# Kernel optimization log

Measured on AMD Instinct MI355X. Metric: run time of the kernel, lower is better.

## Reference

```python
import jax, jax.numpy as jnp
import numpy as np

C = 256  # image_channels == mask_channels == output_channels

def setup_inputs() -> dict:
    key = jax.random.key(0)
    ks = jax.random.split(key, 10)
    B, H, W = 16, 48, 48
    s = 0.02
    return {
        "image_feat": jax.random.normal(ks[0], (B, C, H, W), jnp.float32),
        "mask_feat": jax.random.normal(ks[1], (B, C, H, W), jnp.float32),
        "Wq": jax.random.normal(ks[2], (C, C), jnp.float32) * s,
        "bq": jnp.zeros((C,), jnp.float32),
        "Wk": jax.random.normal(ks[3], (C, C), jnp.float32) * s,
        "bk": jnp.zeros((C,), jnp.float32),
        "Wv": jax.random.normal(ks[4], (C, C), jnp.float32) * s,
        "bv": jnp.zeros((C,), jnp.float32),
        "Wo": jax.random.normal(ks[5], (C, C), jnp.float32) * s,
        "bo": jnp.zeros((C,), jnp.float32),
    }

def reference(image_feat, mask_feat, Wq, bq, Wk, bk, Wv, bv, Wo, bo):
    B, Cc, H, W = image_feat.shape
    N = H * W
    img = image_feat.reshape(B, Cc, N)   # [B, C, N]
    msk = mask_feat.reshape(B, Cc, N)
    # 1x1 convs == per-pixel linear over channels
    q = jnp.einsum('oc,bcn->bon', Wq, msk) + bq[None, :, None]
    k = jnp.einsum('oc,bcn->bon', Wk, img) + bk[None, :, None]
    v = jnp.einsum('oc,bcn->bon', Wv, img) + bv[None, :, None]
    scale = Cc ** (-0.5)
    # attn[b, n, m] = <q[:, n], k[:, m]>
    attn = jnp.einsum('bcn,bcm->bnm', q, k) * scale
    attn = jax.nn.softmax(attn, axis=-1)
    # attended[b, c, n] = sum_m v[b, c, m] * attn[b, n, m]
    av = jnp.einsum('bcm,bnm->bcn', v, attn)
    out = jnp.einsum('oc,bcn->bon', Wo, av) + bo[None, :, None]
    return image_feat + out.reshape(B, Cc, H, W)
```

## Files before the change

kernel.cpp:

```cpp
#include <hip/hip_runtime.h>

#define NBATCH 16
#define CCH 256
#define NTOK 2304

typedef __attribute__((ext_vector_type(8))) short bf16x8;
typedef __attribute__((ext_vector_type(4))) short bf16x4v;
typedef __attribute__((ext_vector_type(4))) float f32x4;

__device__ __forceinline__ short f2bf(float x){
  unsigned u = __builtin_bit_cast(unsigned, x);
  u = u + 0x7FFFu + ((u >> 16) & 1u);
  return (short)(u >> 16);
}
__device__ __forceinline__ float bf2f(short h){
  unsigned u = ((unsigned)(unsigned short)h) << 16;
  return __builtin_bit_cast(float, u);
}

__device__ __forceinline__ void gld_lds16(const short* g, short* l){
  __builtin_amdgcn_global_load_lds((const __attribute__((address_space(1))) void*)g,
                                   (__attribute__((address_space(3))) void*)l, 16, 0, 0);
}

__global__ __launch_bounds__(256) void cw_kernel(const float* __restrict__ Wq, const float* __restrict__ Wk,
                                                 const float* __restrict__ Wv, const float* __restrict__ Wo,
                                                 short* __restrict__ out){
  int idx = blockIdx.x * 256 + threadIdx.x;
  int which = idx >> 14;
  int off = idx & 16383;
  const float* src = which==0 ? Wq : which==1 ? Wk : which==2 ? Wv : Wo;
  float4 v = ((const float4*)src)[off];
  bf16x4v pk = { f2bf(v.x), f2bf(v.y), f2bf(v.z), f2bf(v.w) };
  *(bf16x4v*)(out + ((size_t)which << 16) + ((size_t)off << 2)) = pk;
}

__global__ __launch_bounds__(256) void prep_kernel(const float* __restrict__ img, const float* __restrict__ msk,
                                                   short* __restrict__ imgT, short* __restrict__ mskT){
  int zz = blockIdx.z; int b = zz >> 1; int which = zz & 1;
  const float* src = (which ? msk : img) + (size_t)b * CCH * NTOK;
  short* dst = (which ? mskT : imgT) + (size_t)b * NTOK * CCH;
  int n0 = blockIdx.x * 64, c0 = blockIdx.y * 64;
  __shared__ __align__(16) short tile[64][72];
  int tid = threadIdx.x;
  int r = tid >> 2, g = tid & 3;
  const float* p = src + (size_t)(c0 + r) * NTOK + n0 + 16 * g;
  #pragma unroll
  for (int q4 = 0; q4 < 4; q4++){
    float4 v = *(const float4*)(p + 4 * q4);
    tile[16*g + 4*q4 + 0][r] = f2bf(v.x);
    tile[16*g + 4*q4 + 1][r] = f2bf(v.y);
    tile[16*g + 4*q4 + 2][r] = f2bf(v.z);
    tile[16*g + 4*q4 + 3][r] = f2bf(v.w);
  }
  __syncthreads();
  short* qp = dst + (size_t)(n0 + r) * CCH + c0 + 16 * g;
  *(bf16x8*)qp = *(const bf16x8*)&tile[r][16*g];
  *(bf16x8*)(qp + 8) = *(const bf16x8*)&tile[r][16*g + 8];
}

__device__ __forceinline__ void gemm128(const short* __restrict__ Ablk, const short* __restrict__ Bblk,
                                        short* As, short* Bs, f32x4 (&acc)[4][4]){
  const int tid = threadIdx.x;
  const int l = tid & 63, w = tid >> 6;
  const int l15 = l & 15, lhi = l >> 4;
  const int wi = w >> 1, wj = w & 1;
  const int srow = tid >> 3, scs = tid & 7;
  const f32x4 z4 = {0.f, 0.f, 0.f, 0.f};
  #pragma unroll
  for (int mt = 0; mt < 4; mt++)
    #pragma unroll
    for (int nt = 0; nt < 4; nt++) acc[mt][nt] = z4;

  #pragma unroll 1
  for (int kt = 0; kt < 4; kt++){
    const int k0 = kt * 64;
    bf16x8 ra[4], rb[4];
    #pragma unroll
    for (int p = 0; p < 4; p++){
      const int row = p * 32 + srow;
      ra[p] = *(const bf16x8*)(Ablk + (size_t)row * CCH + k0 + 8 * scs);
      rb[p] = *(const bf16x8*)(Bblk + (size_t)row * CCH + k0 + 8 * scs);
    }
    __syncthreads();
    #pragma unroll
    for (int p = 0; p < 4; p++){
      const int row = p * 32 + srow;
      const int sw = (scs ^ (row & 7)) << 3;
      *(bf16x8*)(As + row * 64 + sw) = ra[p];
      *(bf16x8*)(Bs + row * 64 + sw) = rb[p];
    }
    __syncthreads();
    #pragma unroll
    for (int kk = 0; kk < 2; kk++){
      bf16x8 afr[4], bfr[4];
      #pragma unroll
      for (int mt = 0; mt < 4; mt++){
        const int row = 64 * wi + 16 * mt + l15;
        const int ch = 4 * kk + lhi;
        afr[mt] = *(const bf16x8*)(As + row * 64 + ((ch ^ (row & 7)) << 3));
      }
      #pragma unroll
      for (int nt = 0; nt < 4; nt++){
        const int row = 64 * wj + 16 * nt + l15;
        const int ch = 4 * kk + lhi;
        bfr[nt] = *(const bf16x8*)(Bs + row * 64 + ((ch ^ (row & 7)) << 3));
      }
      #pragma unroll
      for (int mt = 0; mt < 4; mt++)
        #pragma unroll
        for (int nt = 0; nt < 4; nt++)
          acc[mt][nt] = __builtin_amdgcn_mfma_f32_16x16x32_bf16(afr[mt], bfr[nt], acc[mt][nt], 0, 0, 0);
    }
  }
}

__global__ __launch_bounds__(256) void proj_kernel(const short* __restrict__ imgT, const short* __restrict__ mskT,
                                                   const short* __restrict__ Wb,
                                                   const float* __restrict__ bq, const float* __restrict__ bk,
                                                   const float* __restrict__ bv,
                                                   short* __restrict__ Qt, short* __restrict__ Kt,
                                                   short* __restrict__ Vn){
  __shared__ __align__(16) short As[128 * 64];
  __shared__ __align__(16) short Bs[128 * 64];
  const int b = blockIdx.z, which = blockIdx.y, bx = blockIdx.x;
  const size_t nbT = (size_t)b * NTOK * CCH;
  const short* Ablk; const short* Bblk; short* outp; const float* bias;
  int ti, tj, ldout; bool biasRow; float scl;
  if (which == 0){
    ti = bx >> 1; tj = bx & 1;
    Ablk = mskT + nbT + (size_t)ti * 128 * CCH;
    Bblk = Wb + (size_t)tj * 128 * CCH;
    outp = Qt + nbT; bias = bq; ldout = CCH; biasRow = false;
    scl = 0.0625f * 1.44269504088896f;
  } else if (which == 1){
    ti = bx >> 1; tj = bx & 1;
    Ablk = imgT + nbT + (size_t)ti * 128 * CCH;
    Bblk = Wb + 65536 + (size_t)tj * 128 * CCH;
    outp = Kt + nbT; bias = bk; ldout = CCH; biasRow = false; scl = 1.0f;
  } else {
    ti = bx / 18; tj = bx % 18;
    Ablk = Wb + 2 * 65536 + (size_t)ti * 128 * CCH;
    Bblk = imgT + nbT + (size_t)tj * 128 * CCH;
    outp = Vn + nbT; bias = bv; ldout = NTOK; biasRow = true; scl = 1.0f;
  }
  f32x4 acc[4][4];
  gemm128(Ablk, Bblk, As, Bs, acc);
  const int l = threadIdx.x & 63, w = threadIdx.x >> 6;
  const int l15 = l & 15, lhi = l >> 4, wi = w >> 1, wj = w & 1;
  #pragma unroll
  for (int mt = 0; mt < 4; mt++){
    const int i0 = ti * 128 + 64 * wi + 16 * mt + 4 * lhi;
    #pragma unroll
    for (int nt = 0; nt < 4; nt++){
      const int j = tj * 128 + 64 * wj + 16 * nt + l15;
      const float bj = biasRow ? 0.f : bias[j];
      #pragma unroll
      for (int r = 0; r < 4; r++){
        float v = acc[mt][nt][r] + (biasRow ? bias[i0 + r] : bj);
        outp[(size_t)(i0 + r) * ldout + j] = f2bf(v * scl);
      }
    }
  }
}

__global__ __launch_bounds__(256) void attn_kernel(const short* __restrict__ Qt, const short* __restrict__ Kt,
                                                   const short* __restrict__ Vn,
                                                   short* __restrict__ Opart, float* __restrict__ lsumg){
  const int phys = blockIdx.x;
  const int L = (phys & 7) * 144 + (phys >> 3);
  const int b = L / 72;
  const int rem = L % 72;
  const int half = rem / 36;
  const int q0 = (rem % 36) * 64;
  const int t0 = half * 18;
  const int tid = threadIdx.x, w = tid >> 6, l = tid & 63;
  const int l15 = l & 15, lhi = l >> 4;
  const short* Qb = Qt + (size_t)b * NTOK * CCH;
  const short* Kb = Kt + (size_t)b * NTOK * CCH;
  const short* Vb = Vn + (size_t)b * CCH * NTOK;
  __shared__ __align__(16) short Ks[64 * 256];
  __shared__ __align__(16) short P_lds[64 * 64];

  const int st_row = (l >> 5);
  const int st_ch  = (l & 31);

  bf16x8 qf[8];
  {
    const short* qrow = Qb + (size_t)(q0 + 16 * w + l15) * CCH + 8 * lhi;
    #pragma unroll
    for (int kk = 0; kk < 8; kk++) qf[kk] = *(const bf16x8*)(qrow + 32 * kk);
  }
  const f32x4 z4 = {0.f, 0.f, 0.f, 0.f};
  f32x4 oacc[4][4];
  #pragma unroll
  for (int qt = 0; qt < 4; qt++)
    #pragma unroll
    for (int ct = 0; ct < 4; ct++) oacc[qt][ct] = z4;
  float lpart[4] = {0.f, 0.f, 0.f, 0.f};

#define STAGE_K(M0) do { \
    _Pragma("unroll") \
    for (int r = 0; r < 8; r++){ \
      const int slot = 4 * r + w; \
      const int row = 2 * slot + st_row; \
      const int ch = st_ch ^ (row & 7); \
      gld_lds16(Kb + (size_t)((M0) + row) * CCH + (ch << 3), &Ks[slot * 512]); \
    } } while(0)

  STAGE_K(t0 * 64);

  #pragma unroll 1
  for (int t = t0; t < t0 + 18; t++){
    const int m0 = t * 64;
    __syncthreads();

    bf16x8 vfp[8];
    #pragma unroll
    for (int km = 0; km < 2; km++)
      #pragma unroll
      for (int ct = 0; ct < 4; ct++)
        vfp[4 * km + ct] = *(const bf16x8*)(Vb + (size_t)(64 * w + 16 * ct + l15) * NTOK + m0 + 32 * km + 8 * lhi);

    f32x4 sacc[4] = {z4, z4, z4, z4};
    __builtin_amdgcn_s_setprio(1);
    #pragma unroll
    for (int mjb = 0; mjb < 4; mjb++){
      const int row = 16 * mjb + l15;
      const int rsw = row & 7;
      #pragma unroll
      for (int kk = 0; kk < 8; kk++){
        bf16x8 kf = *(const bf16x8*)(Ks + row * 256 + (((4 * kk + lhi) ^ rsw) << 3));
        sacc[mjb] = __builtin_amdgcn_mfma_f32_16x16x32_bf16(qf[kk], kf, sacc[mjb], 0, 0, 0);
      }
    }
    __builtin_amdgcn_s_setprio(0);
    #pragma unroll
    for (int mjb = 0; mjb < 4; mjb++)
      #pragma unroll
      for (int r = 0; r < 4; r++){
        float p = exp2f(sacc[mjb][r]);
        lpart[r] += p;
        const int prow = 16 * w + 4 * lhi + r;
        const int pcol = 16 * mjb + l15;
        P_lds[prow * 64 + ((((pcol >> 3) ^ (prow & 7)) << 3) | (pcol & 7))] = f2bf(p);
      }
    __syncthreads();

    if (t + 1 < t0 + 18) STAGE_K(m0 + 64);

    __builtin_amdgcn_s_setprio(1);
    #pragma unroll
    for (int km = 0; km < 2; km++){
      bf16x8 pf[4];
      #pragma unroll
      for (int qt = 0; qt < 4; qt++){
        const int prow = 16 * qt + l15;
        pf[qt] = *(const bf16x8*)&P_lds[prow * 64 + (((4 * km + lhi) ^ (prow & 7)) << 3)];
      }
      #pragma unroll
      for (int qt = 0; qt < 4; qt++)
        #pragma unroll
        for (int ct = 0; ct < 4; ct++)
          oacc[qt][ct] = __builtin_amdgcn_mfma_f32_16x16x32_bf16(pf[qt], vfp[4 * km + ct], oacc[qt][ct], 0, 0, 0);
    }
    __builtin_amdgcn_s_setprio(0);
  }
#undef STAGE_K

  const size_t hrow = ((size_t)half * NBATCH + b) * NTOK + q0;
  #pragma unroll
  for (int r = 0; r < 4; r++){
    float s = lpart[r];
    s += __shfl_xor(s, 1); s += __shfl_xor(s, 2); s += __shfl_xor(s, 4); s += __shfl_xor(s, 8);
    if (l15 == 0) lsumg[hrow + 16 * w + 4 * lhi + r] = s;
  }
  short* Ob = Opart + hrow * CCH;
  #pragma unroll
  for (int qt = 0; qt < 4; qt++)
    #pragma unroll
    for (int ct = 0; ct < 4; ct++)
      #pragma unroll
      for (int r = 0; r < 4; r++)
        Ob[(size_t)(16 * qt + 4 * lhi + r) * CCH + 64 * w + 16 * ct + l15] = f2bf(oacc[qt][ct][r]);
}

__global__ __launch_bounds__(512, 4) void final_kernel(
    const float* __restrict__ Wo, const float* __restrict__ bo,
    const short* __restrict__ Op, const float* __restrict__ ls,
    const float* __restrict__ img, float* __restrict__ out){
  __shared__ __align__(16) short XL[128 * 72];
  __shared__ __align__(16) short WL[256 * 64];
  const int ti = blockIdx.x, b = blockIdx.y;
  const int n0 = ti * 128;
  const int t = threadIdx.x, wv = t >> 6, l = t & 63;
  const int l15 = l & 15, lhi = l >> 4;
  const int sn = t >> 2, sj = t & 3;
  const int so = t >> 1, sh = t & 1;
  const size_t HS = (size_t)NBATCH * NTOK * CCH;
  const size_t row = (size_t)b * NTOK + n0 + sn;
  const float inv = 1.0f / (ls[row] + ls[(size_t)NBATCH * NTOK + row]);

  const f32x4 z4 = {0.f, 0.f, 0.f, 0.f};
  f32x4 acc[4][4];
  #pragma unroll
  for (int mt = 0; mt < 4; mt++)
    #pragma unroll
    for (int nt = 0; nt < 4; nt++) acc[mt][nt] = z4;

  #pragma unroll 1
  for (int kt = 0; kt < 4; kt++){
    const int c0 = kt * 64;
    bf16x8 a0[2], a1[2];
    #pragma unroll
    for (int j = 0; j < 2; j++){
      const int c = c0 + (2 * sj + j) * 8;
      a0[j] = *(const bf16x8*)(Op + row * CCH + c);
      a1[j] = *(const bf16x8*)(Op + HS + row * CCH + c);
    }
    float4 wreg[8];
    #pragma unroll
    for (int q = 0; q < 8; q++)
      wreg[q] = *(const float4*)(Wo + (size_t)so * CCH + c0 + 32 * sh + 4 * q);
    __syncthreads();
    #pragma unroll
    for (int j = 0; j < 2; j++){
      const int ch = 2 * sj + j;
      bf16x8 cb;
      #pragma unroll
      for (int e = 0; e < 8; e++)
        cb[e] = f2bf((bf2f(a0[j][e]) + bf2f(a1[j][e])) * inv);
      *(bf16x8*)&XL[sn * 72 + ((ch ^ ((sn >> 4) & 7)) << 3)] = cb;
    }
    #pragma unroll
    for (int q = 0; q < 8; q++){
      const int cl = 32 * sh + 4 * q;
      bf16x4v pk = { f2bf(wreg[q].x), f2bf(wreg[q].y), f2bf(wreg[q].z), f2bf(wreg[q].w) };
      *(bf16x4v*)&WL[so * 64 + ((((cl >> 3) ^ (so & 7)) << 3) | (cl & 7))] = pk;
    }
    __syncthreads();
    const int wi = wv & 3, wj = wv >> 2;
    #pragma unroll
    for (int kk = 0; kk < 2; kk++){
      bf16x8 af[4], bf_[4];
      #pragma unroll
      for (int mt = 0; mt < 4; mt++){
        const int o = 64 * wi + 16 * mt + l15;
        af[mt] = *(const bf16x8*)&WL[o * 64 + (((4 * kk + lhi) ^ (o & 7)) << 3)];
      }
      #pragma unroll
      for (int nt = 0; nt < 4; nt++){
        const int n = 64 * wj + 16 * nt + l15;
        bf_[nt] = *(const bf16x8*)&XL[n * 72 + (((4 * kk + lhi) ^ ((n >> 4) & 7)) << 3)];
      }
      #pragma unroll
      for (int mt = 0; mt < 4; mt++)
        #pragma unroll
        for (int nt = 0; nt < 4; nt++)
          acc[mt][nt] = __builtin_amdgcn_mfma_f32_16x16x32_bf16(af[mt], bf_[nt], acc[mt][nt], 0, 0, 0);
    }
  }
  const int wi = wv & 3, wj = wv >> 2;
  const float* imgb = img + (size_t)b * CCH * NTOK;
  float* outb = out + (size_t)b * CCH * NTOK;
  #pragma unroll
  for (int mt = 0; mt < 4; mt++){
    const int ob = 64 * wi + 16 * mt + 4 * lhi;
    #pragma unroll
    for (int nt = 0; nt < 4; nt++){
      const int ng = n0 + 64 * wj + 16 * nt + l15;
      #pragma unroll
      for (int r = 0; r < 4; r++){
        const size_t idx = (size_t)(ob + r) * NTOK + ng;
        outb[idx] = acc[mt][nt][r] + bo[ob + r] + imgb[idx];
      }
    }
  }
}

extern "C" void kernel_launch(void* const* d_in, const int* in_sizes, int n_in,
                              void* d_out, int out_size, void* d_ws, size_t ws_size,
                              hipStream_t stream) {
  const float* img = (const float*)d_in[0];
  const float* msk = (const float*)d_in[1];
  const float* Wq  = (const float*)d_in[2];
  const float* bq  = (const float*)d_in[3];
  const float* Wk  = (const float*)d_in[4];
  const float* bk  = (const float*)d_in[5];
  const float* Wv  = (const float*)d_in[6];
  const float* bv  = (const float*)d_in[7];
  const float* Wo  = (const float*)d_in[8];
  const float* bo  = (const float*)d_in[9];
  float* out = (float*)d_out;

  short* ws = (short*)d_ws;
  const size_t NE = (size_t)NBATCH * NTOK * CCH;
  short* imgT = ws;
  short* mskT = ws + NE;
  short* Qt   = ws + 2 * NE;
  short* Kt   = ws + 3 * NE;
  short* Vn   = ws + 4 * NE;
  short* Wb   = ws + 5 * NE;
  float* lsumg = (float*)(ws + 5 * NE + 4 * 65536);
  short* Op   = ws;

  cw_kernel<<<dim3(256), dim3(256), 0, stream>>>(Wq, Wk, Wv, Wo, Wb);
  prep_kernel<<<dim3(36, 4, 32), dim3(256), 0, stream>>>(img, msk, imgT, mskT);
  proj_kernel<<<dim3(36, 3, 16), dim3(256), 0, stream>>>(imgT, mskT, Wb, bq, bk, bv, Qt, Kt, Vn);
  attn_kernel<<<dim3(1152), dim3(256), 0, stream>>>(Qt, Kt, Vn, Op, lsumg);
  final_kernel<<<dim3(18, 16), dim3(512), 0, stream>>>(Wo, bo, Op, lsumg, img, out);
}
```

Before: 255.7 us.

## Store Q and K in FP8 and use FP8 MFMA for attention scores

The projection kernel now writes Q and K as FP8 bytes instead of bf16, and the attention kernel stages K into LDS as FP8 and computes QK^T with the 16x16x32 FP8 MFMA. The softmax scale moves from the Q projection into the exp2 argument. This halves Q/K memory and LDS traffic and uses the faster FP8 matrix path, at the cost of reduced precision in the attention logits, which may hurt accuracy.

```diff
diff --git a/kernel.cpp b/kernel.cpp
--- a/kernel.cpp
+++ b/kernel.cpp
@@ -17,8 +17,11 @@
   unsigned u = ((unsigned)(unsigned short)h) << 16;
   return __builtin_bit_cast(float, u);
 }
-
-__device__ __forceinline__ void gld_lds16(const short* g, short* l){
+__device__ __forceinline__ unsigned char f2fp8(float v){
+  return (unsigned char)(__builtin_amdgcn_cvt_pk_fp8_f32(v, v, 0, false) & 0xff);
+}
+
+__device__ __forceinline__ void gld_lds16(const void* g, void* l){
   __builtin_amdgcn_global_load_lds((const __attribute__((address_space(1))) void*)g,
                                    (__attribute__((address_space(3))) void*)l, 16, 0, 0);
 }
@@ -119,52 +122,66 @@
                                                    const short* __restrict__ Wb,
                                                    const float* __restrict__ bq, const float* __restrict__ bk,
                                                    const float* __restrict__ bv,
-                                                   short* __restrict__ Qt, short* __restrict__ Kt,
+                                                   unsigned char* __restrict__ Q8, unsigned char* __restrict__ K8,
                                                    short* __restrict__ Vn){
   __shared__ __align__(16) short As[128 * 64];
   __shared__ __align__(16) short Bs[128 * 64];
   const int b = blockIdx.z, which = blockIdx.y, bx = blockIdx.x;
   const size_t nbT = (size_t)b * NTOK * CCH;
-  const short* Ablk; const short* Bblk; short* outp; const float* bias;
-  int ti, tj, ldout; bool biasRow; float scl;
+  const short* Ablk; const short* Bblk; const float* bias;
+  int ti, tj;
   if (which == 0){
     ti = bx >> 1; tj = bx & 1;
     Ablk = mskT + nbT + (size_t)ti * 128 * CCH;
     Bblk = Wb + (size_t)tj * 128 * CCH;
-    outp = Qt + nbT; bias = bq; ldout = CCH; biasRow = false;
-    scl = 0.0625f * 1.44269504088896f;
+    bias = bq;
   } else if (which == 1){
     ti = bx >> 1; tj = bx & 1;
     Ablk = imgT + nbT + (size_t)ti * 128 * CCH;
     Bblk = Wb + 65536 + (size_t)tj * 128 * CCH;
-    outp = Kt + nbT; bias = bk; ldout = CCH; biasRow = false; scl = 1.0f;
+    bias = bk;
   } else {
     ti = bx / 18; tj = bx % 18;
     Ablk = Wb + 2 * 65536 + (size_t)ti * 128 * CCH;
     Bblk = imgT + nbT + (size_t)tj * 128 * CCH;
-    outp = Vn + nbT; bias = bv; ldout = NTOK; biasRow = true; scl = 1.0f;
+    bias = bv;
   }
   f32x4 acc[4][4];
   gemm128(Ablk, Bblk, As, Bs, acc);
   const int l = threadIdx.x & 63, w = threadIdx.x >> 6;
   const int l15 = l & 15, lhi = l >> 4, wi = w >> 1, wj = w & 1;
-  #pragma unroll
-  for (int mt = 0; mt < 4; mt++){
-    const int i0 = ti * 128 + 64 * wi + 16 * mt + 4 * lhi;
-    #pragma unroll
-    for (int nt = 0; nt < 4; nt++){
-      const int j = tj * 128 + 64 * wj + 16 * nt + l15;
-      const float bj = biasRow ? 0.f : bias[j];
-      #pragma unroll
-      for (int r = 0; r < 4; r++){
-        float v = acc[mt][nt][r] + (biasRow ? bias[i0 + r] : bj);
-        outp[(size_t)(i0 + r) * ldout + j] = f2bf(v * scl);
-      }
-    }
-  }
-}
-
-__global__ __launch_bounds__(256) void attn_kernel(const short* __restrict__ Qt, const short* __restrict__ Kt,
+  if (which < 2){
+    unsigned char* o8 = (which == 0 ? Q8 : K8) + nbT;
+    #pragma unroll
+    for (int mt = 0; mt < 4; mt++){
+      const int i0 = ti * 128 + 64 * wi + 16 * mt + 4 * lhi;
+      #pragma unroll
+      for (int nt = 0; nt < 4; nt++){
+        const int j = tj * 128 + 64 * wj + 16 * nt + l15;
+        const float bj = bias[j];
+        #pragma unroll
+        for (int r = 0; r < 4; r++)
+          o8[(size_t)(i0 + r) * CCH + j] = f2fp8(acc[mt][nt][r] + bj);
+      }
+    }
+  } else {
+    short* outp = Vn + nbT;
+    #pragma unroll
+    for (int mt = 0; mt < 4; mt++){
+      const int i0 = ti * 128 + 64 * wi + 16 * mt + 4 * lhi;
+      #pragma unroll
+      for (int nt = 0; nt < 4; nt++){
+        const int j = tj * 128 + 64 * wj + 16 * nt + l15;
+        #pragma unroll
+        for (int r = 0; r < 4; r++)
+          outp[(size_t)(i0 + r) * NTOK + j] = f2bf(acc[mt][nt][r] + bias[i0 + r]);
+      }
+    }
+  }
+}
+
+__global__ __launch_bounds__(256) void attn_kernel(const unsigned char* __restrict__ Q8,
+                                                   const unsigned char* __restrict__ K8,
                                                    const short* __restrict__ Vn,
                                                    short* __restrict__ Opart, float* __restrict__ lsumg){
   const int phys = blockIdx.x;
@@ -176,20 +193,20 @@
   const int t0 = half * 18;
   const int tid = threadIdx.x, w = tid >> 6, l = tid & 63;
   const int l15 = l & 15, lhi = l >> 4;
-  const short* Qb = Qt + (size_t)b * NTOK * CCH;
-  const short* Kb = Kt + (size_t)b * NTOK * CCH;
+  const unsigned char* Qb = Q8 + (size_t)b * NTOK * CCH;
+  const unsigned char* Kb = K8 + (size_t)b * NTOK * CCH;
   const short* Vb = Vn + (size_t)b * CCH * NTOK;
-  __shared__ __align__(16) short Ks[64 * 256];
+  __shared__ __align__(16) unsigned char Ks8[64 * 256];
   __shared__ __align__(16) short P_lds[64 * 64];
 
-  const int st_row = (l >> 5);
-  const int st_ch  = (l & 31);
-
-  bf16x8 qf[8];
+  const float SCL = 0.0625f * 1.44269504088896f;
+  const int rs2 = (l15 & 7) << 1;
+
+  long qf[8];
   {
-    const short* qrow = Qb + (size_t)(q0 + 16 * w + l15) * CCH + 8 * lhi;
-    #pragma unroll
-    for (int kk = 0; kk < 8; kk++) qf[kk] = *(const bf16x8*)(qrow + 32 * kk);
+    const unsigned char* qrow = Qb + (size_t)(q0 + 16 * w + l15) * CCH + 8 * lhi;
+    #pragma unroll
+    for (int kk = 0; kk < 8; kk++) qf[kk] = *(const long*)(qrow + 32 * kk);
   }
   const f32x4 z4 = {0.f, 0.f, 0.f, 0.f};
   f32x4 oacc[4][4];
@@ -201,11 +218,11 @@
 
 #define STAGE_K(M0) do { \
     _Pragma("unroll") \
-    for (int r = 0; r < 8; r++){ \
+    for (int r = 0; r < 4; r++){ \
       const int slot = 4 * r + w; \
-      const int row = 2 * slot + st_row; \
-      const int ch = st_ch ^ (row & 7); \
-      gld_lds16(Kb + (size_t)((M0) + row) * CCH + (ch << 3), &Ks[slot * 512]); \
+      const int row = 4 * slot + (l >> 4); \
+      const int c16 = (l & 15) ^ (row & 7); \
+      gld_lds16(Kb + (size_t)((M0) + row) * CCH + (c16 << 4), &Ks8[slot * 1024]); \
     } } while(0)
 
   STAGE_K(t0 * 64);
@@ -227,11 +244,11 @@
     #pragma unroll
     for (int mjb = 0; mjb < 4; mjb++){
       const int row = 16 * mjb + l15;
-      const int rsw = row & 7;
       #pragma unroll
       for (int kk = 0; kk < 8; kk++){
-        bf16x8 kf = *(const bf16x8*)(Ks + row * 256 + (((4 * kk + lhi) ^ rsw) << 3));
-        sacc[mjb] = __builtin_amdgcn_mfma_f32_16x16x32_bf16(qf[kk], kf, sacc[mjb], 0, 0, 0);
+        const int c8 = (4 * kk + lhi) ^ rs2;
+        long kf = *(const long*)(Ks8 + row * 256 + (c8 << 3));
+        sacc[mjb] = __builtin_amdgcn_mfma_f32_16x16x32_fp8_fp8(qf[kk], kf, sacc[mjb], 0, 0, 0);
       }
     }
     __builtin_amdgcn_s_setprio(0);
@@ -239,7 +256,7 @@
     for (int mjb = 0; mjb < 4; mjb++)
       #pragma unroll
       for (int r = 0; r < 4; r++){
-        float p = exp2f(sacc[mjb][r]);
+        float p = exp2f(sacc[mjb][r] * SCL);
         lpart[r] += p;
         const int prow = 16 * w + 4 * lhi + r;
         const int pcol = 16 * mjb + l15;
@@ -393,20 +410,20 @@
   const float* bo  = (const float*)d_in[9];
   float* out = (float*)d_out;
 
-  short* ws = (short*)d_ws;
+  char* wsb = (char*)d_ws;
   const size_t NE = (size_t)NBATCH * NTOK * CCH;
-  short* imgT = ws;
-  short* mskT = ws + NE;
-  short* Qt   = ws + 2 * NE;
-  short* Kt   = ws + 3 * NE;
-  short* Vn   = ws + 4 * NE;
-  short* Wb   = ws + 5 * NE;
-  float* lsumg = (float*)(ws + 5 * NE + 4 * 65536);
-  short* Op   = ws;
+  short* imgT = (short*)wsb;
+  short* mskT = (short*)(wsb + 2 * NE);
+  unsigned char* Q8 = (unsigned char*)(wsb + 4 * NE);
+  unsigned char* K8 = (unsigned char*)(wsb + 5 * NE);
+  short* Vn = (short*)(wsb + 6 * NE);
+  short* Wb = (short*)(wsb + 8 * NE);
+  float* lsumg = (float*)(wsb + 8 * NE + 4 * 65536 * 2);
+  short* Op = (short*)wsb;
 
   cw_kernel<<<dim3(256), dim3(256), 0, stream>>>(Wq, Wk, Wv, Wo, Wb);
   prep_kernel<<<dim3(36, 4, 32), dim3(256), 0, stream>>>(img, msk, imgT, mskT);
-  proj_kernel<<<dim3(36, 3, 16), dim3(256), 0, stream>>>(imgT, mskT, Wb, bq, bk, bv, Qt, Kt, Vn);
-  attn_kernel<<<dim3(1152), dim3(256), 0, stream>>>(Qt, Kt, Vn, Op, lsumg);
+  proj_kernel<<<dim3(36, 3, 16), dim3(256), 0, stream>>>(imgT, mskT, Wb, bq, bk, bv, Q8, K8, Vn);
+  attn_kernel<<<dim3(1152), dim3(256), 0, stream>>>(Q8, K8, Vn, Op, lsumg);
   final_kernel<<<dim3(18, 16), dim3(512), 0, stream>>>(Wo, bo, Op, lsumg, img, out);
 }
```

Result: faster. 229.3 us, median of 2 (-10.3%).
